# Performance work log

Measured on AMD Instinct MI355X. Metric: run time of the kernel, lower is better.

Reference implementation:

```python
import jax, jax.numpy as jnp
import numpy as np

INPUT_SIZE = 32
HIDDEN = 64


def _lstm_layer(x, W_ih, W_hh, b_ih, b_hh):
    """Single LSTM layer, batch_first x: (B, T, D) -> (B, T, H).
    PyTorch gate order: i, f, g, o."""
    B, T, _ = x.shape
    H = W_hh.shape[1]
    # Precompute input contribution for all timesteps (the big GEMM).
    xg = jnp.einsum('btd,gd->btg', x, W_ih) + b_ih + b_hh  # (B, T, 4H)
    xg = jnp.swapaxes(xg, 0, 1)  # (T, B, 4H) for scan over time

    def step(carry, g_t):
        h, c = carry
        gates = g_t + h @ W_hh.T  # (B, 4H)
        i, f, g, o = jnp.split(gates, 4, axis=-1)
        c = jax.nn.sigmoid(f) * c + jax.nn.sigmoid(i) * jnp.tanh(g)
        h = jax.nn.sigmoid(o) * jnp.tanh(c)
        return (h, c), h

    h0 = jnp.zeros((B, H), dtype=x.dtype)
    c0 = jnp.zeros((B, H), dtype=x.dtype)
    (_, _), hs = jax.lax.scan(step, (h0, c0), xg)
    return jnp.swapaxes(hs, 0, 1)  # (B, T, H)


def setup_inputs() -> dict:
    key = jax.random.key(0)
    ks = jax.random.split(key, 11)
    B, T, D, H = 1024, 512, INPUT_SIZE, HIDDEN
    s_ih0 = 1.0 / np.sqrt(H)
    u = lambda k, shape: jax.random.uniform(k, shape, jnp.float32, -s_ih0, s_ih0)
    return {
        'x': jax.random.normal(ks[0], (B, T, D), jnp.float32),
        'W_ih0': u(ks[1], (4 * H, D)),
        'W_hh0': u(ks[2], (4 * H, H)),
        'b_ih0': u(ks[3], (4 * H,)),
        'b_hh0': u(ks[4], (4 * H,)),
        'W_ih1': u(ks[5], (4 * H, H)),
        'W_hh1': u(ks[6], (4 * H, H)),
        'b_ih1': u(ks[7], (4 * H,)),
        'b_hh1': u(ks[8], (4 * H,)),
        'W_fc': u(ks[9], (1, H)),
        'b_fc': u(ks[10], (1,)),
    }


def reference(x, W_ih0, W_hh0, b_ih0, b_hh0, W_ih1, W_hh1, b_ih1, b_hh1, W_fc, b_fc):
    h1 = _lstm_layer(x, W_ih0, W_hh0, b_ih0, b_hh0)   # (B, T, H)
    h2 = _lstm_layer(h1, W_ih1, W_hh1, b_ih1, b_hh1)  # (B, T, H)
    last = h2[:, -1, :]                                # (B, H)
    return last @ W_fc.T + b_fc                        # (B, 1)
```

## Files before the change

kernel.cpp:

```cpp
#include <hip/hip_runtime.h>

#define T_STEPS 512

typedef __attribute__((ext_vector_type(8))) short s16x8;
typedef __attribute__((ext_vector_type(4))) float f32x4;

__device__ __forceinline__ short f2bf(float v) {
    unsigned u = __float_as_uint(v);
    return (short)((u + 0x7FFFu + ((u >> 16) & 1u)) >> 16);
}
__device__ __forceinline__ float bf2f(short b) {
    return __uint_as_float(((unsigned)(unsigned short)b) << 16);
}
#define LOG2E 1.4426950408889634f
__device__ __forceinline__ float rcpf(float x)  { return __builtin_amdgcn_rcpf(x); }
__device__ __forceinline__ float ex2f(float x)  { return __builtin_amdgcn_exp2f(x); }
__device__ __forceinline__ float sigf(float x)  { return rcpf(1.f + ex2f(-LOG2E * x)); }
__device__ __forceinline__ float tanhf_(float x){ return 1.f - 2.f * rcpf(ex2f(2.f * LOG2E * x) + 1.f); }

#define BAR() do { asm volatile("s_waitcnt lgkmcnt(0)" ::: "memory"); \
                   __builtin_amdgcn_s_barrier(); } while (0)

__global__ __launch_bounds__(512, 2)
void lstm2_mfma(const float* __restrict__ x,
                const float* __restrict__ Wih0, const float* __restrict__ Whh0,
                const float* __restrict__ bih0, const float* __restrict__ bhh0,
                const float* __restrict__ Wih1, const float* __restrict__ Whh1,
                const float* __restrict__ bih1, const float* __restrict__ bhh1,
                const float* __restrict__ Wfc,  const float* __restrict__ bfc,
                float* __restrict__ out)
{
    __shared__ __align__(16) short bB[2][4][176];
    __shared__ __align__(16) float gbuf0[256 * 4];
    __shared__ __align__(16) float gbuf1[256 * 4];

    const int tid  = threadIdx.x;
    const int w    = tid >> 6;
    const int lane = tid & 63;
    const int n16  = lane & 15;
    const int q4   = lane >> 4;
    const int b0   = blockIdx.x * 4;

    s16x8 a0[2], a1[2], a2[2];
    s16x8 e0[2], e1[2], e2[2], e3[2];
    f32x4 bias0[2], bias1[2];
#pragma unroll
    for (int t = 0; t < 2; ++t) {
        const int rowW = (n16 & 3) * 64 + 8 * w + 4 * t + (n16 >> 2);
#pragma unroll
        for (int j = 0; j < 8; ++j) {
            a0[t][j] = f2bf(Wih0[rowW * 32 + q4 * 8 + j]);
            a1[t][j] = f2bf(Whh0[rowW * 64 + q4 * 8 + j]);
            a2[t][j] = f2bf(Whh0[rowW * 64 + 32 + q4 * 8 + j]);
            e0[t][j] = f2bf(Wih1[rowW * 64 + q4 * 8 + j]);
            e1[t][j] = f2bf(Wih1[rowW * 64 + 32 + q4 * 8 + j]);
            e2[t][j] = f2bf(Whh1[rowW * 64 + q4 * 8 + j]);
            e3[t][j] = f2bf(Whh1[rowW * 64 + 32 + q4 * 8 + j]);
        }
        const int jl = 8 * w + 4 * t + q4;
#pragma unroll
        for (int p_ = 0; p_ < 4; ++p_) {
            bias0[t][p_] = bih0[p_ * 64 + jl] + bhh0[p_ * 64 + jl];
            bias1[t][p_] = bih1[p_ * 64 + jl] + bhh1[p_ * 64 + jl];
        }
    }

    const int gw0 = ((8 * w + q4) * 4 + n16) * 4;
    const int gw1 = ((8 * w + 4 + q4) * 4 + n16) * 4;
    const int cw  = w & 3;
    const int cs  = 16 * cw + (lane >> 2);
    const int cb  = lane & 3;
    const int gri = 64 * cw + lane;

    const int nB  = (n16 < 4) ? n16 : 3;

    const bool isx = (w < 2);
    const int  xb  = w * 2 + (lane >> 5);
    const int  xk  = lane & 31;
    const float* xp = x + ((size_t)(b0 + xb) * T_STEPS) * 32 + xk;

    for (int i = tid; i < 2 * 4 * 176 / 2; i += 512) ((int*)bB)[i] = 0;
    __syncthreads();
    float xc = 0.f;
    if (isx) {
        bB[0][xb][xk] = f2bf(xp[0]);
        xc = xp[32];
    }
    __syncthreads();

    float cst0 = 0.f, cst1 = 0.f;

    for (int it = 0; it <= T_STEPS; ++it) {
        const int p = it & 1;

        if (isx && it + 1 < T_STEPS) bB[p ^ 1][xb][xk] = f2bf(xc);
        float xn = 0.f;
        if (isx && it + 2 < T_STEPS) xn = xp[(size_t)(it + 2) * 32];

        const short* bp = &bB[p][nB][q4 * 8];
        s16x8 t0 = *(const s16x8*)(bp);
        s16x8 t1 = *(const s16x8*)(bp + 32);
        s16x8 t2 = *(const s16x8*)(bp + 64);
        s16x8 t3 = *(const s16x8*)(bp + 96);
        s16x8 t4 = *(const s16x8*)(bp + 128);

        f32x4 d0a = __builtin_amdgcn_mfma_f32_16x16x32_bf16(a0[0], t0, bias0[0], 0, 0, 0);
        f32x4 d0b = __builtin_amdgcn_mfma_f32_16x16x32_bf16(a0[1], t0, bias0[1], 0, 0, 0);
        d0a = __builtin_amdgcn_mfma_f32_16x16x32_bf16(a1[0], t1, d0a, 0, 0, 0);
        d0b = __builtin_amdgcn_mfma_f32_16x16x32_bf16(a1[1], t1, d0b, 0, 0, 0);
        d0a = __builtin_amdgcn_mfma_f32_16x16x32_bf16(a2[0], t2, d0a, 0, 0, 0);
        d0b = __builtin_amdgcn_mfma_f32_16x16x32_bf16(a2[1], t2, d0b, 0, 0, 0);

        f32x4 d1a = __builtin_amdgcn_mfma_f32_16x16x32_bf16(e0[0], t1, bias1[0], 0, 0, 0);
        f32x4 d1b = __builtin_amdgcn_mfma_f32_16x16x32_bf16(e0[1], t1, bias1[1], 0, 0, 0);
        d1a = __builtin_amdgcn_mfma_f32_16x16x32_bf16(e1[0], t2, d1a, 0, 0, 0);
        d1b = __builtin_amdgcn_mfma_f32_16x16x32_bf16(e1[1], t2, d1b, 0, 0, 0);
        d1a = __builtin_amdgcn_mfma_f32_16x16x32_bf16(e2[0], t3, d1a, 0, 0, 0);
        d1b = __builtin_amdgcn_mfma_f32_16x16x32_bf16(e2[1], t3, d1b, 0, 0, 0);
        d1a = __builtin_amdgcn_mfma_f32_16x16x32_bf16(e3[0], t4, d1a, 0, 0, 0);
        d1b = __builtin_amdgcn_mfma_f32_16x16x32_bf16(e3[1], t4, d1b, 0, 0, 0);

        if (n16 < 4) {
            *(f32x4*)&gbuf0[gw0] = d0a;
            *(f32x4*)&gbuf0[gw1] = d0b;
            *(f32x4*)&gbuf1[gw0] = d1a;
            *(f32x4*)&gbuf1[gw1] = d1b;
        }
        BAR();

        if (w < 4) {
            if (it < T_STEPS) {
                f32x4 g = *(const f32x4*)&gbuf0[gri * 4];
                float cc = sigf(g[1]) * cst0 + sigf(g[0]) * tanhf_(g[2]);
                cst0 = cc;
                bB[p ^ 1][cb][32 + cs] = f2bf(sigf(g[3]) * tanhf_(cc));
            }
        } else {
            if (it >= 1) {
                f32x4 g = *(const f32x4*)&gbuf1[gri * 4];
                float cc = sigf(g[1]) * cst1 + sigf(g[0]) * tanhf_(g[2]);
                cst1 = cc;
                bB[p ^ 1][cb][96 + cs] = f2bf(sigf(g[3]) * tanhf_(cc));
            }
        }
        BAR();
        xc = xn;
    }

    if (tid < 4) {
        float s = bfc[0];
#pragma unroll
        for (int k = 0; k < 64; ++k)
            s += bf2f(bB[1][tid][96 + k]) * Wfc[k];
        out[b0 + tid] = s;
    }
}

extern "C" void kernel_launch(void* const* d_in, const int* in_sizes, int n_in,
                              void* d_out, int out_size, void* d_ws, size_t ws_size,
                              hipStream_t stream) {
    const float* x    = (const float*)d_in[0];
    const float* Wih0 = (const float*)d_in[1];
    const float* Whh0 = (const float*)d_in[2];
    const float* bih0 = (const float*)d_in[3];
    const float* bhh0 = (const float*)d_in[4];
    const float* Wih1 = (const float*)d_in[5];
    const float* Whh1 = (const float*)d_in[6];
    const float* bih1 = (const float*)d_in[7];
    const float* bhh1 = (const float*)d_in[8];
    const float* Wfc  = (const float*)d_in[9];
    const float* bfc  = (const float*)d_in[10];
    float* out = (float*)d_out;

    const int B = out_size;
    dim3 grid(B / 4), block(512);
    hipLaunchKernelGGL(lstm2_mfma, grid, block, 0, stream,
                       x, Wih0, Whh0, bih0, bhh0,
                       Wih1, Whh1, bih1, bhh1, Wfc, bfc, out);
}
```

Measured before the change: 478.7 us.

## Specialize waves per LSTM layer instead of splitting gate rows across all waves

Waves 0-3 now compute only the layer-0 gate GEMM and waves 4-7 only the layer-1 gate GEMM, each covering 16 hidden units across four MFMA accumulators. Before, every wave did both layers for 8 hidden units. Each wave now keeps one layer's weights in registers and issues 12 or 16 MFMAs per step instead of 14, with longer independent accumulator chains. The two wave groups carry unequal MFMA work, so the group-1 waves may end up on the critical path at each barrier.

```diff
diff --git a/kernel.cpp b/kernel.cpp
--- a/kernel.cpp
+++ b/kernel.cpp
@@ -40,37 +40,44 @@
     const int n16  = lane & 15;
     const int q4   = lane >> 4;
     const int b0   = blockIdx.x * 4;
-
-    s16x8 a0[2], a1[2], a2[2];
-    s16x8 e0[2], e1[2], e2[2], e3[2];
-    f32x4 bias0[2], bias1[2];
-#pragma unroll
-    for (int t = 0; t < 2; ++t) {
-        const int rowW = (n16 & 3) * 64 + 8 * w + 4 * t + (n16 >> 2);
-#pragma unroll
-        for (int j = 0; j < 8; ++j) {
-            a0[t][j] = f2bf(Wih0[rowW * 32 + q4 * 8 + j]);
-            a1[t][j] = f2bf(Whh0[rowW * 64 + q4 * 8 + j]);
-            a2[t][j] = f2bf(Whh0[rowW * 64 + 32 + q4 * 8 + j]);
-            e0[t][j] = f2bf(Wih1[rowW * 64 + q4 * 8 + j]);
-            e1[t][j] = f2bf(Wih1[rowW * 64 + 32 + q4 * 8 + j]);
-            e2[t][j] = f2bf(Whh1[rowW * 64 + q4 * 8 + j]);
-            e3[t][j] = f2bf(Whh1[rowW * 64 + 32 + q4 * 8 + j]);
+    const bool gA  = (w < 4);
+    const int wg   = w & 3;
+
+    s16x8 af[16];
+    f32x4 bias[4];
+#pragma unroll
+    for (int t = 0; t < 4; ++t) {
+        const int rowW = (n16 & 3) * 64 + 16 * wg + 4 * t + (n16 >> 2);
+        if (gA) {
+#pragma unroll
+            for (int j = 0; j < 8; ++j) {
+                af[t * 3 + 0][j] = f2bf(Wih0[rowW * 32 + q4 * 8 + j]);
+                af[t * 3 + 1][j] = f2bf(Whh0[rowW * 64 + q4 * 8 + j]);
+                af[t * 3 + 2][j] = f2bf(Whh0[rowW * 64 + 32 + q4 * 8 + j]);
+            }
+        } else {
+#pragma unroll
+            for (int j = 0; j < 8; ++j) {
+                af[t * 4 + 0][j] = f2bf(Wih1[rowW * 64 + q4 * 8 + j]);
+                af[t * 4 + 1][j] = f2bf(Wih1[rowW * 64 + 32 + q4 * 8 + j]);
+                af[t * 4 + 2][j] = f2bf(Whh1[rowW * 64 + q4 * 8 + j]);
+                af[t * 4 + 3][j] = f2bf(Whh1[rowW * 64 + 32 + q4 * 8 + j]);
+            }
         }
-        const int jl = 8 * w + 4 * t + q4;
-#pragma unroll
-        for (int p_ = 0; p_ < 4; ++p_) {
-            bias0[t][p_] = bih0[p_ * 64 + jl] + bhh0[p_ * 64 + jl];
-            bias1[t][p_] = bih1[p_ * 64 + jl] + bhh1[p_ * 64 + jl];
-        }
-    }
-
-    const int gw0 = ((8 * w + q4) * 4 + n16) * 4;
-    const int gw1 = ((8 * w + 4 + q4) * 4 + n16) * 4;
-    const int cw  = w & 3;
-    const int cs  = 16 * cw + (lane >> 2);
+        const int jl = 16 * wg + 4 * t + q4;
+        const float* bi = gA ? bih0 : bih1;
+        const float* bh = gA ? bhh0 : bhh1;
+#pragma unroll
+        for (int p_ = 0; p_ < 4; ++p_)
+            bias[t][p_] = bi[p_ * 64 + jl] + bh[p_ * 64 + jl];
+    }
+
+    int gw[4];
+#pragma unroll
+    for (int t = 0; t < 4; ++t) gw[t] = ((16 * wg + 4 * t + q4) * 4 + n16) * 4;
+    const int cs  = 16 * wg + (lane >> 2);
     const int cb  = lane & 3;
-    const int gri = 64 * cw + lane;
+    const int gri = 64 * wg + lane;
 
     const int nB  = (n16 < 4) ? n16 : 3;
 
@@ -88,7 +95,7 @@
     }
     __syncthreads();
 
-    float cst0 = 0.f, cst1 = 0.f;
+    float cst = 0.f;
 
     for (int it = 0; it <= T_STEPS; ++it) {
         const int p = it & 1;
@@ -98,48 +105,71 @@
         if (isx && it + 2 < T_STEPS) xn = xp[(size_t)(it + 2) * 32];
 
         const short* bp = &bB[p][nB][q4 * 8];
-        s16x8 t0 = *(const s16x8*)(bp);
-        s16x8 t1 = *(const s16x8*)(bp + 32);
-        s16x8 t2 = *(const s16x8*)(bp + 64);
-        s16x8 t3 = *(const s16x8*)(bp + 96);
-        s16x8 t4 = *(const s16x8*)(bp + 128);
-
-        f32x4 d0a = __builtin_amdgcn_mfma_f32_16x16x32_bf16(a0[0], t0, bias0[0], 0, 0, 0);
-        f32x4 d0b = __builtin_amdgcn_mfma_f32_16x16x32_bf16(a0[1], t0, bias0[1], 0, 0, 0);
-        d0a = __builtin_amdgcn_mfma_f32_16x16x32_bf16(a1[0], t1, d0a, 0, 0, 0);
-        d0b = __builtin_amdgcn_mfma_f32_16x16x32_bf16(a1[1], t1, d0b, 0, 0, 0);
-        d0a = __builtin_amdgcn_mfma_f32_16x16x32_bf16(a2[0], t2, d0a, 0, 0, 0);
-        d0b = __builtin_amdgcn_mfma_f32_16x16x32_bf16(a2[1], t2, d0b, 0, 0, 0);
-
-        f32x4 d1a = __builtin_amdgcn_mfma_f32_16x16x32_bf16(e0[0], t1, bias1[0], 0, 0, 0);
-        f32x4 d1b = __builtin_amdgcn_mfma_f32_16x16x32_bf16(e0[1], t1, bias1[1], 0, 0, 0);
-        d1a = __builtin_amdgcn_mfma_f32_16x16x32_bf16(e1[0], t2, d1a, 0, 0, 0);
-        d1b = __builtin_amdgcn_mfma_f32_16x16x32_bf16(e1[1], t2, d1b, 0, 0, 0);
-        d1a = __builtin_amdgcn_mfma_f32_16x16x32_bf16(e2[0], t3, d1a, 0, 0, 0);
-        d1b = __builtin_amdgcn_mfma_f32_16x16x32_bf16(e2[1], t3, d1b, 0, 0, 0);
-        d1a = __builtin_amdgcn_mfma_f32_16x16x32_bf16(e3[0], t4, d1a, 0, 0, 0);
-        d1b = __builtin_amdgcn_mfma_f32_16x16x32_bf16(e3[1], t4, d1b, 0, 0, 0);
-
-        if (n16 < 4) {
-            *(f32x4*)&gbuf0[gw0] = d0a;
-            *(f32x4*)&gbuf0[gw1] = d0b;
-            *(f32x4*)&gbuf1[gw0] = d1a;
-            *(f32x4*)&gbuf1[gw1] = d1b;
+        f32x4 dd0, dd1, dd2, dd3;
+        if (gA) {
+            s16x8 t0 = *(const s16x8*)(bp);
+            s16x8 t1 = *(const s16x8*)(bp + 32);
+            s16x8 t2 = *(const s16x8*)(bp + 64);
+            dd0 = __builtin_amdgcn_mfma_f32_16x16x32_bf16(af[0],  t0, bias[0], 0, 0, 0);
+            dd1 = __builtin_amdgcn_mfma_f32_16x16x32_bf16(af[3],  t0, bias[1], 0, 0, 0);
+            dd2 = __builtin_amdgcn_mfma_f32_16x16x32_bf16(af[6],  t0, bias[2], 0, 0, 0);
+            dd3 = __builtin_amdgcn_mfma_f32_16x16x32_bf16(af[9],  t0, bias[3], 0, 0, 0);
+            dd0 = __builtin_amdgcn_mfma_f32_16x16x32_bf16(af[1],  t1, dd0, 0, 0, 0);
+            dd1 = __builtin_amdgcn_mfma_f32_16x16x32_bf16(af[4],  t1, dd1, 0, 0, 0);
+            dd2 = __builtin_amdgcn_mfma_f32_16x16x32_bf16(af[7],  t1, dd2, 0, 0, 0);
+            dd3 = __builtin_amdgcn_mfma_f32_16x16x32_bf16(af[10], t1, dd3, 0, 0, 0);
+            dd0 = __builtin_amdgcn_mfma_f32_16x16x32_bf16(af[2],  t2, dd0, 0, 0, 0);
+            dd1 = __builtin_amdgcn_mfma_f32_16x16x32_bf16(af[5],  t2, dd1, 0, 0, 0);
+            dd2 = __builtin_amdgcn_mfma_f32_16x16x32_bf16(af[8],  t2, dd2, 0, 0, 0);
+            dd3 = __builtin_amdgcn_mfma_f32_16x16x32_bf16(af[11], t2, dd3, 0, 0, 0);
+            if (n16 < 4) {
+                *(f32x4*)&gbuf0[gw[0]] = dd0;
+                *(f32x4*)&gbuf0[gw[1]] = dd1;
+                *(f32x4*)&gbuf0[gw[2]] = dd2;
+                *(f32x4*)&gbuf0[gw[3]] = dd3;
+            }
+        } else {
+            s16x8 t1 = *(const s16x8*)(bp + 32);
+            s16x8 t2 = *(const s16x8*)(bp + 64);
+            s16x8 t3 = *(const s16x8*)(bp + 96);
+            s16x8 t4 = *(const s16x8*)(bp + 128);
+            dd0 = __builtin_amdgcn_mfma_f32_16x16x32_bf16(af[0],  t1, bias[0], 0, 0, 0);
+            dd1 = __builtin_amdgcn_mfma_f32_16x16x32_bf16(af[4],  t1, bias[1], 0, 0, 0);
+            dd2 = __builtin_amdgcn_mfma_f32_16x16x32_bf16(af[8],  t1, bias[2], 0, 0, 0);
+            dd3 = __builtin_amdgcn_mfma_f32_16x16x32_bf16(af[12], t1, bias[3], 0, 0, 0);
+            dd0 = __builtin_amdgcn_mfma_f32_16x16x32_bf16(af[1],  t2, dd0, 0, 0, 0);
+            dd1 = __builtin_amdgcn_mfma_f32_16x16x32_bf16(af[5],  t2, dd1, 0, 0, 0);
+            dd2 = __builtin_amdgcn_mfma_f32_16x16x32_bf16(af[9],  t2, dd2, 0, 0, 0);
+            dd3 = __builtin_amdgcn_mfma_f32_16x16x32_bf16(af[13], t2, dd3, 0, 0, 0);
+            dd0 = __builtin_amdgcn_mfma_f32_16x16x32_bf16(af[2],  t3, dd0, 0, 0, 0);
+            dd1 = __builtin_amdgcn_mfma_f32_16x16x32_bf16(af[6],  t3, dd1, 0, 0, 0);
+            dd2 = __builtin_amdgcn_mfma_f32_16x16x32_bf16(af[10], t3, dd2, 0, 0, 0);
+            dd3 = __builtin_amdgcn_mfma_f32_16x16x32_bf16(af[14], t3, dd3, 0, 0, 0);
+            dd0 = __builtin_amdgcn_mfma_f32_16x16x32_bf16(af[3],  t4, dd0, 0, 0, 0);
+            dd1 = __builtin_amdgcn_mfma_f32_16x16x32_bf16(af[7],  t4, dd1, 0, 0, 0);
+            dd2 = __builtin_amdgcn_mfma_f32_16x16x32_bf16(af[11], t4, dd2, 0, 0, 0);
+            dd3 = __builtin_amdgcn_mfma_f32_16x16x32_bf16(af[15], t4, dd3, 0, 0, 0);
+            if (n16 < 4) {
+                *(f32x4*)&gbuf1[gw[0]] = dd0;
+                *(f32x4*)&gbuf1[gw[1]] = dd1;
+                *(f32x4*)&gbuf1[gw[2]] = dd2;
+                *(f32x4*)&gbuf1[gw[3]] = dd3;
+            }
         }
         BAR();
 
-        if (w < 4) {
+        if (gA) {
             if (it < T_STEPS) {
                 f32x4 g = *(const f32x4*)&gbuf0[gri * 4];
-                float cc = sigf(g[1]) * cst0 + sigf(g[0]) * tanhf_(g[2]);
-                cst0 = cc;
+                float cc = sigf(g[1]) * cst + sigf(g[0]) * tanhf_(g[2]);
+                cst = cc;
                 bB[p ^ 1][cb][32 + cs] = f2bf(sigf(g[3]) * tanhf_(cc));
             }
         } else {
             if (it >= 1) {
                 f32x4 g = *(const f32x4*)&gbuf1[gri * 4];
-                float cc = sigf(g[1]) * cst1 + sigf(g[0]) * tanhf_(g[2]);
-                cst1 = cc;
+                float cc = sigf(g[1]) * cst + sigf(g[0]) * tanhf_(g[2]);
+                cst = cc;
                 bB[p ^ 1][cb][96 + cs] = f2bf(sigf(g[3]) * tanhf_(cc));
             }
         }
```

New measurement: 490.4 us. 2.5% more time.
